# Kernel tuning notes

Hardware: AMD Instinct MI355X
Metric: run time of the kernel (lower is better)

## Reference

```python
import jax, jax.numpy as jnp
import numpy as np

N, E = 100000, 1600000
F_IN, H, HG, L, C = 128, 128, 128, 3, 40


def setup_inputs() -> dict:
    key = jax.random.key(0)
    ks = jax.random.split(key, 12)
    s = 0.05
    return dict(
        x=jax.random.normal(ks[0], (N, F_IN), jnp.float32),
        edge_index=jax.random.randint(ks[1], (2, E), 0, N),
        edge_weight=jax.random.uniform(ks[2], (E,), jnp.float32),
        h0=jax.random.normal(ks[3], (N, HG), jnp.float32),
        linW=jax.random.normal(ks[4], (F_IN, H), jnp.float32) * s,
        linB=jnp.zeros((H,), jnp.float32),
        convW=jax.random.normal(ks[5], (L, H, H), jnp.float32) * s,
        convB=jnp.zeros((L, H), jnp.float32),
        gru_Wih=jax.random.normal(ks[6], (3 * HG, H), jnp.float32) * s,
        gru_Whh=jax.random.normal(ks[7], (3 * HG, HG), jnp.float32) * s,
        gru_bih=jnp.zeros((3 * HG,), jnp.float32),
        gru_bhh=jnp.zeros((3 * HG,), jnp.float32),
        fcW=jax.random.normal(ks[8], (HG, C), jnp.float32) * s,
        fcB=jnp.zeros((C,), jnp.float32),
    )


def _gru(x, h, Wih, Whh, bih, bhh):
    # torch.nn.GRUCell math (gate order: r, z, n)
    gi = x @ Wih.T + bih  # [N, 3*HG]
    gh = h @ Whh.T + bhh  # [N, 3*HG]
    ir, iz, in_ = jnp.split(gi, 3, axis=-1)
    hr, hz, hn = jnp.split(gh, 3, axis=-1)
    r = jax.nn.sigmoid(ir + hr)
    z = jax.nn.sigmoid(iz + hz)
    n = jnp.tanh(in_ + r * hn)
    return (1.0 - z) * n + z * h


def _gcn_conv(x, src, dst, ew, W, b, n_nodes):
    # PyG GCNConv: linear -> symmetric-normalized sparse aggregation -> bias
    xw = x @ W  # [N, H]
    deg = jax.ops.segment_sum(ew, dst, num_segments=n_nodes)
    dinv = jnp.where(deg > 0, jax.lax.rsqrt(deg), 0.0)
    norm = dinv[src] * ew * dinv[dst]  # [E+N]
    msg = xw[src] * norm[:, None]      # gather + scale (irregular access)
    out = jax.ops.segment_sum(msg, dst, num_segments=n_nodes)  # scatter-add
    return out + b


def reference(x, edge_index, edge_weight, h0, linW, linB, convW, convB,
              gru_Wih, gru_Whh, gru_bih, gru_bhh, fcW, fcB):
    n_nodes = x.shape[0]
    # GCNConv default: add self-loops with weight 1 before normalization
    loops = jnp.arange(n_nodes)
    src = jnp.concatenate([edge_index[0], loops])
    dst = jnp.concatenate([edge_index[1], loops])
    ew = jnp.concatenate([edge_weight, jnp.ones((n_nodes,), edge_weight.dtype)])

    h = h0
    xh = jax.nn.relu(x @ linW + linB)
    h = _gru(xh, h, gru_Wih, gru_Whh, gru_bih, gru_bhh)
    for l in range(convW.shape[0]):  # fixed small layer count
        xh = jax.nn.relu(_gcn_conv(xh, src, dst, ew, convW[l], convB[l], n_nodes))
        h = _gru(xh, h, gru_Wih, gru_Whh, gru_bih, gru_bhh)
    return h @ fcW + fcB
```

## Files before the change

### kernel.cpp

```cpp
#include <hip/hip_runtime.h>
#include <hip/hip_bf16.h>
#include <math.h>

typedef __attribute__((ext_vector_type(8))) short bf8_t;
typedef __attribute__((ext_vector_type(4))) float f4_t;
typedef __attribute__((ext_vector_type(8))) unsigned short us8_t;

__device__ inline unsigned short f2bf(float f) {
  union { float f; unsigned u; } x; x.f = f;
  unsigned r = x.u + 0x7FFF + ((x.u >> 16) & 1);
  return (unsigned short)(r >> 16);
}
__device__ inline float bf2f(unsigned short b) {
  union { unsigned u; float f; } x; x.u = ((unsigned)b) << 16;
  return x.f;
}
__device__ inline float bflo(unsigned v) {
  union { unsigned u; float f; } x; x.u = v << 16; return x.f;
}
__device__ inline float bfhi(unsigned v) {
  union { unsigned u; float f; } x; x.u = v & 0xFFFF0000u; return x.f;
}

__device__ inline void async_copy16(const void* g, void* l) {
  __builtin_amdgcn_global_load_lds(
      (const __attribute__((address_space(1))) unsigned int*)g,
      (__attribute__((address_space(3))) unsigned int*)l, 16, 0, 0);
}


__global__ void k_zero_i(int* __restrict__ p, int n) {
  int i = blockIdx.x * blockDim.x + threadIdx.x;
  if (i < n) p[i] = 0;
}

__global__ void k_count_pos(const int* __restrict__ dst, int* __restrict__ cnt,
                            int* __restrict__ pos, int E) {
  int e = blockIdx.x * blockDim.x + threadIdx.x;
  if (e < E) pos[e] = atomicAdd(&cnt[dst[e]], 1);
}

__global__ void k_f2bf(const float* __restrict__ in, unsigned short* __restrict__ out,
                       size_t n8) {
  size_t i = (size_t)blockIdx.x * blockDim.x + threadIdx.x;
  if (i >= n8) return;
  const float4* p = (const float4*)(in + i * 8);
  float4 a = p[0], b = p[1];
  us8_t v;
  v[0] = f2bf(a.x); v[1] = f2bf(a.y); v[2] = f2bf(a.z); v[3] = f2bf(a.w);
  v[4] = f2bf(b.x); v[5] = f2bf(b.y); v[6] = f2bf(b.z); v[7] = f2bf(b.w);
  *(us8_t*)(out + i * 8) = v;
}

__global__ void k_packB(const float* __restrict__ W, unsigned short* __restrict__ out,
                        int K, int Ncols, int ldw, int trans) {
  int idx = blockIdx.x * 256 + threadIdx.x;
  int total = (Ncols / 16) * (K / 32) * 64;
  if (idx >= total) return;
  int lane = idx & 63;
  int frag = idx >> 6;
  int kt = K / 32;
  int k0 = frag % kt;
  int n0 = frag / kt;
  int n = n0 * 16 + (lane & 15);
  int kbase = k0 * 32 + (lane >> 4) * 8;
  us8_t v;
#pragma unroll
  for (int j = 0; j < 8; ++j) {
    int k = kbase + j;
    float f = trans ? W[(size_t)n * ldw + k] : W[(size_t)k * ldw + n];
    v[j] = f2bf(f);
  }
  *(us8_t*)(out + (size_t)idx * 8) = v;
}


__global__ __launch_bounds__(256) void k_scan_block(
    const int* __restrict__ cnt, int* __restrict__ partial,
    int* __restrict__ bsum, int n) {
  __shared__ int s[256];
  int tid = threadIdx.x;
  int i = blockIdx.x * 256 + tid;
  s[tid] = (i < n) ? cnt[i] : 0;
  __syncthreads();
#pragma unroll
  for (int d = 1; d < 256; d <<= 1) {
    int t = (tid >= d) ? s[tid - d] : 0;
    __syncthreads();
    s[tid] += t;
    __syncthreads();
  }
  if (i < n) partial[i] = s[tid];
  if (tid == 255) bsum[blockIdx.x] = s[255];
}

__global__ __launch_bounds__(512) void k_scan_sums(int* __restrict__ bsum, int nb) {
  __shared__ int s[512];
  int tid = threadIdx.x;
  s[tid] = (tid < nb) ? bsum[tid] : 0;
  __syncthreads();
#pragma unroll
  for (int d = 1; d < 512; d <<= 1) {
    int t = (tid >= d) ? s[tid - d] : 0;
    __syncthreads();
    s[tid] += t;
    __syncthreads();
  }
  if (tid < nb) bsum[tid] = s[tid];
}

__global__ __launch_bounds__(256) void k_scan_add(
    const int* __restrict__ partial, const int* __restrict__ bsum,
    int* __restrict__ rowptr, int n) {
  int i = blockIdx.x * 256 + threadIdx.x;
  if (i == 0) rowptr[0] = 0;
  if (i < n) {
    int v = partial[i] + (blockIdx.x > 0 ? bsum[blockIdx.x - 1] : 0);
    rowptr[i + 1] = v;
  }
}

__global__ __launch_bounds__(256) void k_csr_fill(
    const int* __restrict__ src, const int* __restrict__ dst,
    const float* __restrict__ ew, const int* __restrict__ rowptr,
    const int* __restrict__ pos, int2* __restrict__ csr, int E) {
  int e = blockIdx.x * 256 + threadIdx.x;
  if (e >= E) return;
  int d = dst[e];
  int p = rowptr[d] + pos[e];
  csr[p] = make_int2(src[e], __float_as_int(ew[e]));
}

__global__ __launch_bounds__(256) void k_deg_dinv(
    const int* __restrict__ rowptr, const int2* __restrict__ csr,
    float* __restrict__ dinv, int N) {
  int n = blockIdx.x * 256 + threadIdx.x;
  if (n >= N) return;
  int b = rowptr[n], e = rowptr[n + 1];
  float s = 1.0f;
  for (int j = b; j < e; ++j) s += __int_as_float(csr[j].y);
  dinv[n] = rsqrtf(s);
}

__global__ __launch_bounds__(256) void k_norm_csr(
    const int* __restrict__ rowptr, int2* __restrict__ csr,
    const float* __restrict__ dinv, int N) {
  int n = blockIdx.x * 256 + threadIdx.x;
  if (n >= N) return;
  int b = rowptr[n], e = rowptr[n + 1];
  float dn = dinv[n];
  for (int j = b; j < e; ++j) {
    int2 t = csr[j];
    float w = dinv[t.x] * __int_as_float(t.y) * dn;
    csr[j] = make_int2(t.x, __float_as_int(w));
  }
}


template<bool RELU, bool BIAS>
__global__ __launch_bounds__(256) void k_mfma_gemm(
    const unsigned short* __restrict__ A, const unsigned short* __restrict__ Bp,
    const float* __restrict__ bias, unsigned short* __restrict__ C, int M) {
  __shared__ unsigned char smem[32 * 1024];
  int wave = threadIdx.x >> 6, lane = threadIdx.x & 63;
  int row0 = (blockIdx.x * 4 + wave) * 16;
  int m = lane & 15, q = lane >> 4;

#pragma unroll
  for (int i = 0; i < 8; ++i) {
    int f = wave * 8 + i;
    async_copy16((const unsigned char*)Bp + (size_t)f * 1024 + lane * 16,
                 smem + f * 1024);
  }
  __syncthreads();
  if (row0 >= M) return;

  int arow = row0 + m; if (arow >= M) arow = M - 1;
  bf8_t a[4];
#pragma unroll
  for (int k0 = 0; k0 < 4; ++k0)
    a[k0] = *(const bf8_t*)(A + (size_t)arow * 128 + k0 * 32 + q * 8);

#pragma unroll
  for (int n0 = 0; n0 < 8; ++n0) {
    f4_t acc = {};
#pragma unroll
    for (int k0 = 0; k0 < 4; ++k0) {
      bf8_t b = *(const bf8_t*)(smem + (n0 * 4 + k0) * 1024 + lane * 16);
      acc = __builtin_amdgcn_mfma_f32_16x16x32_bf16(a[k0], b, acc, 0, 0, 0);
    }
    int col = n0 * 16 + m;
    float bs = BIAS ? bias[col] : 0.f;
#pragma unroll
    for (int r = 0; r < 4; ++r) {
      int grow = row0 + q * 4 + r;
      if (grow < M) {
        float v = acc[r] + bs;
        if (RELU) v = fmaxf(v, 0.f);
        C[(size_t)grow * 128 + col] = f2bf(v);
      }
    }
  }
}


__global__ __launch_bounds__(256) void k_gru_mfma(
    const unsigned short* __restrict__ xh,
    const float* h_in,
    float* h_out,
    const unsigned short* __restrict__ Bi,
    const unsigned short* __restrict__ Bh,
    const float* __restrict__ bih, const float* __restrict__ bhh, int M) {
  __shared__ unsigned char smem[24 * 1024];
  int wave = threadIdx.x >> 6, lane = threadIdx.x & 63;
  int row0 = (blockIdx.x * 4 + wave) * 16;
  int m = lane & 15, q = lane >> 4;
  int arow = row0 + m; if (arow >= M) arow = M - 1;

  bf8_t ax[4], ah[4];
#pragma unroll
  for (int k0 = 0; k0 < 4; ++k0) {
    ax[k0] = *(const bf8_t*)(xh + (size_t)arow * 128 + k0 * 32 + q * 8);
    const float* hp = h_in + (size_t)arow * 128 + k0 * 32 + q * 8;
    float4 h0 = *(const float4*)hp;
    float4 h1 = *(const float4*)(hp + 4);
    bf8_t t;
    t[0] = (short)f2bf(h0.x); t[1] = (short)f2bf(h0.y);
    t[2] = (short)f2bf(h0.z); t[3] = (short)f2bf(h0.w);
    t[4] = (short)f2bf(h1.x); t[5] = (short)f2bf(h1.y);
    t[6] = (short)f2bf(h1.z); t[7] = (short)f2bf(h1.w);
    ah[k0] = t;
  }

  auto stage = [&](int g) {
#pragma unroll
    for (int s = 0; s < 6; ++s) {
      int cc = g + 8 * (s >= 3 ? s - 3 : s);
      const unsigned short* src = (s < 3) ? Bi : Bh;
      int f = s * 4 + wave;
      async_copy16((const unsigned char*)src + ((size_t)(cc * 4 + wave)) * 1024 + lane * 16,
                   smem + f * 1024);
    }
  };

  stage(0);
  for (int g = 0; g < 8; ++g) {
    __syncthreads();
    f4_t air = {}, aiz = {}, ain = {}, ahr = {}, ahz = {}, ahn = {};
#pragma unroll
    for (int k0 = 0; k0 < 4; ++k0) {
      bf8_t br = *(const bf8_t*)(smem + (0 * 4 + k0) * 1024 + lane * 16);
      bf8_t bz = *(const bf8_t*)(smem + (1 * 4 + k0) * 1024 + lane * 16);
      bf8_t bn = *(const bf8_t*)(smem + (2 * 4 + k0) * 1024 + lane * 16);
      bf8_t cr = *(const bf8_t*)(smem + (3 * 4 + k0) * 1024 + lane * 16);
      bf8_t cz = *(const bf8_t*)(smem + (4 * 4 + k0) * 1024 + lane * 16);
      bf8_t cn = *(const bf8_t*)(smem + (5 * 4 + k0) * 1024 + lane * 16);
      air = __builtin_amdgcn_mfma_f32_16x16x32_bf16(ax[k0], br, air, 0, 0, 0);
      aiz = __builtin_amdgcn_mfma_f32_16x16x32_bf16(ax[k0], bz, aiz, 0, 0, 0);
      ain = __builtin_amdgcn_mfma_f32_16x16x32_bf16(ax[k0], bn, ain, 0, 0, 0);
      ahr = __builtin_amdgcn_mfma_f32_16x16x32_bf16(ah[k0], cr, ahr, 0, 0, 0);
      ahz = __builtin_amdgcn_mfma_f32_16x16x32_bf16(ah[k0], cz, ahz, 0, 0, 0);
      ahn = __builtin_amdgcn_mfma_f32_16x16x32_bf16(ah[k0], cn, ahn, 0, 0, 0);
    }
    __syncthreads();
    if (g < 7) stage(g + 1);

    int col = g * 16 + m;
    float bir_ = bih[col], biz_ = bih[col + 128], bin_ = bih[col + 256];
    float bhr_ = bhh[col], bhz_ = bhh[col + 128], bhn_ = bhh[col + 256];
#pragma unroll
    for (int r = 0; r < 4; ++r) {
      int grow = row0 + q * 4 + r;
      if (grow < M) {
        float hprev = h_in[(size_t)grow * 128 + col];
        float rr = 1.f / (1.f + expf(-(air[r] + bir_ + ahr[r] + bhr_)));
        float zz = 1.f / (1.f + expf(-(aiz[r] + biz_ + ahz[r] + bhz_)));
        float nn = tanhf(ain[r] + bin_ + rr * (ahn[r] + bhn_));
        h_out[(size_t)grow * 128 + col] = (1.f - zz) * nn + zz * hprev;
      }
    }
  }
}


template<bool RELU, bool BIAS>
__global__ __launch_bounds__(256) void k_gemm128(
    const float* __restrict__ A, const float* __restrict__ B,
    const float* __restrict__ bias, float* __restrict__ C, int M, int Nc) {
  __shared__ float As[64][36];
  __shared__ float Bs[32][64];
  int tid = threadIdx.x;
  int tx = tid & 15, ty = tid >> 4;
  int row0 = blockIdx.y * 64, col0 = blockIdx.x * 64;
  float acc[4][4] = {};

  for (int k0 = 0; k0 < 128; k0 += 32) {
#pragma unroll
    for (int i = 0; i < 2; ++i) {
      int f = tid + i * 256;
      int r = f >> 3, c4 = f & 7;
      int gr = row0 + r;
      float4 v = make_float4(0.f, 0.f, 0.f, 0.f);
      if (gr < M) v = *(const float4*)(A + (size_t)gr * 128 + k0 + c4 * 4);
      *(float4*)(&As[r][c4 * 4]) = v;
    }
#pragma unroll
    for (int i = 0; i < 2; ++i) {
      int f = tid + i * 256;
      int r = f >> 4, c4 = f & 15;
      int gc = col0 + c4 * 4;
      float4 v = make_float4(0.f, 0.f, 0.f, 0.f);
      if (gc + 3 < Nc) v = *(const float4*)(B + (size_t)(k0 + r) * Nc + gc);
      *(float4*)(&Bs[r][c4 * 4]) = v;
    }
    __syncthreads();
#pragma unroll
    for (int kk = 0; kk < 32; ++kk) {
      float4 b = *(float4*)(&Bs[kk][tx * 4]);
      float a0 = As[ty * 4 + 0][kk];
      float a1 = As[ty * 4 + 1][kk];
      float a2 = As[ty * 4 + 2][kk];
      float a3 = As[ty * 4 + 3][kk];
      acc[0][0] += a0 * b.x; acc[0][1] += a0 * b.y; acc[0][2] += a0 * b.z; acc[0][3] += a0 * b.w;
      acc[1][0] += a1 * b.x; acc[1][1] += a1 * b.y; acc[1][2] += a1 * b.z; acc[1][3] += a1 * b.w;
      acc[2][0] += a2 * b.x; acc[2][1] += a2 * b.y; acc[2][2] += a2 * b.z; acc[2][3] += a2 * b.w;
      acc[3][0] += a3 * b.x; acc[3][1] += a3 * b.y; acc[3][2] += a3 * b.z; acc[3][3] += a3 * b.w;
    }
    __syncthreads();
  }

#pragma unroll
  for (int i = 0; i < 4; ++i) {
    int gr = row0 + ty * 4 + i;
    if (gr >= M) continue;
#pragma unroll
    for (int j = 0; j < 4; ++j) {
      int gc = col0 + tx * 4 + j;
      if (gc >= Nc) continue;
      float v = acc[i][j];
      if (BIAS) v += bias[gc];
      if (RELU) v = fmaxf(v, 0.f);
      C[(size_t)gr * Nc + gc] = v;
    }
  }
}


__global__ __launch_bounds__(256) void k_gather(
    const int* __restrict__ rowptr, const int2* __restrict__ csr,
    const unsigned* __restrict__ xw,
    const float* __restrict__ dinv, const float* __restrict__ bias,
    unsigned* __restrict__ out, int N) {
  int wave = threadIdx.x >> 6;
  int lane = threadIdx.x & 63;
  int node = __builtin_amdgcn_readfirstlane(blockIdx.x * 4 + wave);
  if (node >= N) return;
  int beg = __builtin_amdgcn_readfirstlane(rowptr[node]);
  int end = __builtin_amdgcn_readfirstlane(rowptr[node + 1]);

  float accl = 0.f, acch = 0.f;
  int k = beg;
  for (; k + 4 <= end; k += 4) {
    int2 e0 = csr[k], e1 = csr[k + 1], e2 = csr[k + 2], e3 = csr[k + 3];
    unsigned v0 = xw[((size_t)e0.x << 6) + lane];
    unsigned v1 = xw[((size_t)e1.x << 6) + lane];
    unsigned v2 = xw[((size_t)e2.x << 6) + lane];
    unsigned v3 = xw[((size_t)e3.x << 6) + lane];
    float w0 = __int_as_float(e0.y), w1 = __int_as_float(e1.y);
    float w2 = __int_as_float(e2.y), w3 = __int_as_float(e3.y);
    accl += bflo(v0) * w0; acch += bfhi(v0) * w0;
    accl += bflo(v1) * w1; acch += bfhi(v1) * w1;
    accl += bflo(v2) * w2; acch += bfhi(v2) * w2;
    accl += bflo(v3) * w3; acch += bfhi(v3) * w3;
  }
  for (; k < end; ++k) {
    int2 e = csr[k];
    unsigned v = xw[((size_t)e.x << 6) + lane];
    float w = __int_as_float(e.y);
    accl += bflo(v) * w; acch += bfhi(v) * w;
  }

  float di = dinv[node];
  float sn = di * di;
  unsigned vs = xw[((size_t)node << 6) + lane];
  float2 b = *(const float2*)(bias + lane * 2);
  float rl = fmaxf(accl + bflo(vs) * sn + b.x, 0.f);
  float rh = fmaxf(acch + bfhi(vs) * sn + b.y, 0.f);
  unsigned o = (unsigned)f2bf(rl) | ((unsigned)f2bf(rh) << 16);
  out[((size_t)node << 6) + lane] = o;
}


extern "C" void kernel_launch(void* const* d_in, const int* in_sizes, int n_in,
                              void* d_out, int out_size, void* d_ws, size_t ws_size,
                              hipStream_t stream) {
  const float* x    = (const float*)d_in[0];
  const int*   ei   = (const int*)d_in[1];
  const float* ew   = (const float*)d_in[2];
  const float* h0   = (const float*)d_in[3];
  const float* linW = (const float*)d_in[4];
  const float* linB = (const float*)d_in[5];
  const float* convW= (const float*)d_in[6];
  const float* convB= (const float*)d_in[7];
  const float* Wih  = (const float*)d_in[8];
  const float* Whh  = (const float*)d_in[9];
  const float* bih  = (const float*)d_in[10];
  const float* bhh  = (const float*)d_in[11];
  const float* fcW  = (const float*)d_in[12];
  const float* fcB  = (const float*)d_in[13];

  int N = in_sizes[0] / 128;
  int E = in_sizes[1] / 2;
  const int* srcI = ei;
  const int* dstI = ei + E;
  int nb = (N + 255) / 256;

  float* ws = (float*)d_ws;
  size_t off = 0;
  float* dinv = ws + off; off += (size_t)N;
  if (off & 1) off++;
  float* h    = ws + off; off += (size_t)N * 128;
  int* iws = (int*)(ws + off);
  size_t ioff = 0;
  int2* csr    = (int2*)iws; ioff += (size_t)2 * E;
  int* cnt     = iws + ioff; ioff += (size_t)N;
  int* partial = iws + ioff; ioff += (size_t)N;
  int* bsum    = iws + ioff; ioff += 512;
  int* rowptr  = iws + ioff; ioff += (size_t)N + 1;
  ioff = (ioff + 3) & ~(size_t)3;
  unsigned short* usws = (unsigned short*)(iws + ioff);
  size_t uoff = 0;
  unsigned short* x_bf   = usws + uoff; uoff += (size_t)N * 128;
  unsigned short* xh_bf  = usws + uoff; uoff += (size_t)N * 128;
  unsigned short* xw_bf  = usws + uoff; uoff += (size_t)N * 128;
  unsigned short* linWp  = usws + uoff; uoff += 128 * 128;
  unsigned short* convWp = usws + uoff; uoff += 3 * 128 * 128;
  unsigned short* Bi     = usws + uoff; uoff += 384 * 128;
  unsigned short* Bh     = usws + uoff; uoff += 384 * 128;

  int* pos = (int*)xw_bf;

  k_packB<<<(8 * 4 * 64 + 255) / 256, 256, 0, stream>>>(linW, linWp, 128, 128, 128, 0);
  for (int l = 0; l < 3; ++l)
    k_packB<<<(8 * 4 * 64 + 255) / 256, 256, 0, stream>>>(
        convW + (size_t)l * 128 * 128, convWp + (size_t)l * 128 * 128, 128, 128, 128, 0);
  k_packB<<<(24 * 4 * 64 + 255) / 256, 256, 0, stream>>>(Wih, Bi, 128, 384, 128, 1);
  k_packB<<<(24 * 4 * 64 + 255) / 256, 256, 0, stream>>>(Whh, Bh, 128, 384, 128, 1);

  k_f2bf<<<(int)(((size_t)N * 16 + 255) / 256), 256, 0, stream>>>(x, x_bf, (size_t)N * 16);

  k_zero_i<<<nb, 256, 0, stream>>>(cnt, N);
  k_count_pos<<<(E + 255) / 256, 256, 0, stream>>>(dstI, cnt, pos, E);
  k_scan_block<<<nb, 256, 0, stream>>>(cnt, partial, bsum, N);
  k_scan_sums<<<1, 512, 0, stream>>>(bsum, nb);
  k_scan_add<<<nb, 256, 0, stream>>>(partial, bsum, rowptr, N);
  k_csr_fill<<<(E + 255) / 256, 256, 0, stream>>>(
      srcI, dstI, ew, rowptr, pos, csr, E);

  k_deg_dinv<<<nb, 256, 0, stream>>>(rowptr, csr, dinv, N);
  k_norm_csr<<<nb, 256, 0, stream>>>(rowptr, csr, dinv, N);

  int gwave = (N + 63) / 64;

  k_mfma_gemm<true, true><<<gwave, 256, 0, stream>>>(x_bf, linWp, linB, xh_bf, N);

  k_gru_mfma<<<gwave, 256, 0, stream>>>(xh_bf, h0, h, Bi, Bh, bih, bhh, N);

  int ggat = (N + 3) / 4;
  for (int l = 0; l < 3; ++l) {
    k_mfma_gemm<false, false><<<gwave, 256, 0, stream>>>(
        xh_bf, convWp + (size_t)l * 128 * 128, nullptr, xw_bf, N);
    k_gather<<<ggat, 256, 0, stream>>>(
        rowptr, csr, (const unsigned*)xw_bf, dinv, convB + (size_t)l * 128,
        (unsigned*)xh_bf, N);
    k_gru_mfma<<<gwave, 256, 0, stream>>>(xh_bf, h, h, Bi, Bh, bih, bhh, N);
  }

  dim3 g40(1, (N + 63) / 64);
  k_gemm128<false, true><<<g40, 256, 0, stream>>>(h, fcW, fcB, (float*)d_out, N, 40);
}
```

Measured before the change: 914.2 us.

## Fuse gather with GRU and merge independent setup kernels by block-range dispatch

The sparse aggregation is fused into the GRU kernel. Each wave gathers 16 nodes, writes the bf16 rows into swizzled LDS, and feeds them straight to the MFMA GRU, so the xh round trip through global memory disappears and the last layer skips writing xh entirely. Independent setup steps (weight packing with count zeroing, edge counting with f32-to-bf16 conversion, CSR fill with the input linear, degree with the first GRU, normalisation with the first conv GEMM) are merged into single launches that split work by block index. CSR accesses also switch to nontemporal loads and stores. The gather now runs serially over 16 nodes per wave instead of one node per wave, which cuts parallelism and latency hiding in the irregular gather phase.

```diff
diff --git a/kernel.cpp b/kernel.cpp
--- a/kernel.cpp
+++ b/kernel.cpp
@@ -11,10 +11,6 @@
   unsigned r = x.u + 0x7FFF + ((x.u >> 16) & 1);
   return (unsigned short)(r >> 16);
 }
-__device__ inline float bf2f(unsigned short b) {
-  union { unsigned u; float f; } x; x.u = ((unsigned)b) << 16;
-  return x.f;
-}
 __device__ inline float bflo(unsigned v) {
   union { unsigned u; float f; } x; x.u = v << 16; return x.f;
 }
@@ -29,32 +25,10 @@
 }
 
 
-__global__ void k_zero_i(int* __restrict__ p, int n) {
-  int i = blockIdx.x * blockDim.x + threadIdx.x;
-  if (i < n) p[i] = 0;
-}
-
-__global__ void k_count_pos(const int* __restrict__ dst, int* __restrict__ cnt,
-                            int* __restrict__ pos, int E) {
-  int e = blockIdx.x * blockDim.x + threadIdx.x;
-  if (e < E) pos[e] = atomicAdd(&cnt[dst[e]], 1);
-}
-
-__global__ void k_f2bf(const float* __restrict__ in, unsigned short* __restrict__ out,
-                       size_t n8) {
-  size_t i = (size_t)blockIdx.x * blockDim.x + threadIdx.x;
-  if (i >= n8) return;
-  const float4* p = (const float4*)(in + i * 8);
-  float4 a = p[0], b = p[1];
-  us8_t v;
-  v[0] = f2bf(a.x); v[1] = f2bf(a.y); v[2] = f2bf(a.z); v[3] = f2bf(a.w);
-  v[4] = f2bf(b.x); v[5] = f2bf(b.y); v[6] = f2bf(b.z); v[7] = f2bf(b.w);
-  *(us8_t*)(out + i * 8) = v;
-}
-
-__global__ void k_packB(const float* __restrict__ W, unsigned short* __restrict__ out,
-                        int K, int Ncols, int ldw, int trans) {
-  int idx = blockIdx.x * 256 + threadIdx.x;
+__device__ inline void packB_body(const float* __restrict__ W,
+                                  unsigned short* __restrict__ out,
+                                  int K, int Ncols, int ldw, int trans, int bid) {
+  int idx = bid * 256 + threadIdx.x;
   int total = (Ncols / 16) * (K / 32) * 64;
   if (idx >= total) return;
   int lane = idx & 63;
@@ -74,96 +48,55 @@
   *(us8_t*)(out + (size_t)idx * 8) = v;
 }
 
-
-__global__ __launch_bounds__(256) void k_scan_block(
-    const int* __restrict__ cnt, int* __restrict__ partial,
-    int* __restrict__ bsum, int n) {
-  __shared__ int s[256];
-  int tid = threadIdx.x;
-  int i = blockIdx.x * 256 + tid;
-  s[tid] = (i < n) ? cnt[i] : 0;
-  __syncthreads();
-#pragma unroll
-  for (int d = 1; d < 256; d <<= 1) {
-    int t = (tid >= d) ? s[tid - d] : 0;
-    __syncthreads();
-    s[tid] += t;
-    __syncthreads();
-  }
-  if (i < n) partial[i] = s[tid];
-  if (tid == 255) bsum[blockIdx.x] = s[255];
-}
-
-__global__ __launch_bounds__(512) void k_scan_sums(int* __restrict__ bsum, int nb) {
-  __shared__ int s[512];
-  int tid = threadIdx.x;
-  s[tid] = (tid < nb) ? bsum[tid] : 0;
-  __syncthreads();
-#pragma unroll
-  for (int d = 1; d < 512; d <<= 1) {
-    int t = (tid >= d) ? s[tid - d] : 0;
-    __syncthreads();
-    s[tid] += t;
-    __syncthreads();
-  }
-  if (tid < nb) bsum[tid] = s[tid];
-}
-
-__global__ __launch_bounds__(256) void k_scan_add(
-    const int* __restrict__ partial, const int* __restrict__ bsum,
-    int* __restrict__ rowptr, int n) {
-  int i = blockIdx.x * 256 + threadIdx.x;
-  if (i == 0) rowptr[0] = 0;
-  if (i < n) {
-    int v = partial[i] + (blockIdx.x > 0 ? bsum[blockIdx.x - 1] : 0);
-    rowptr[i + 1] = v;
-  }
-}
-
-__global__ __launch_bounds__(256) void k_csr_fill(
-    const int* __restrict__ src, const int* __restrict__ dst,
-    const float* __restrict__ ew, const int* __restrict__ rowptr,
-    const int* __restrict__ pos, int2* __restrict__ csr, int E) {
-  int e = blockIdx.x * 256 + threadIdx.x;
+__device__ inline void fill_body(const int* __restrict__ src, const int* __restrict__ dst,
+                                 const float* __restrict__ ew, const int* __restrict__ rowptr,
+                                 const int* __restrict__ pos, int2* __restrict__ csr,
+                                 int E, int bid) {
+  int e = bid * 256 + threadIdx.x;
   if (e >= E) return;
   int d = dst[e];
   int p = rowptr[d] + pos[e];
-  csr[p] = make_int2(src[e], __float_as_int(ew[e]));
-}
-
-__global__ __launch_bounds__(256) void k_deg_dinv(
-    const int* __restrict__ rowptr, const int2* __restrict__ csr,
-    float* __restrict__ dinv, int N) {
-  int n = blockIdx.x * 256 + threadIdx.x;
+  unsigned long long v = (unsigned long long)(unsigned)src[e] |
+                         ((unsigned long long)(unsigned)__float_as_int(ew[e]) << 32);
+  __builtin_nontemporal_store(v, (unsigned long long*)(csr + p));
+}
+
+__device__ inline void deg_body(const int* __restrict__ rowptr, const int2* __restrict__ csr,
+                                float* __restrict__ dinv, int N, int bid) {
+  int n = bid * 256 + threadIdx.x;
   if (n >= N) return;
   int b = rowptr[n], e = rowptr[n + 1];
   float s = 1.0f;
-  for (int j = b; j < e; ++j) s += __int_as_float(csr[j].y);
+  for (int j = b; j < e; ++j) {
+    unsigned long long v = __builtin_nontemporal_load((const unsigned long long*)(csr + j));
+    s += __int_as_float((int)(v >> 32));
+  }
   dinv[n] = rsqrtf(s);
 }
 
-__global__ __launch_bounds__(256) void k_norm_csr(
-    const int* __restrict__ rowptr, int2* __restrict__ csr,
-    const float* __restrict__ dinv, int N) {
-  int n = blockIdx.x * 256 + threadIdx.x;
+__device__ inline void norm_body(const int* __restrict__ rowptr, int2* __restrict__ csr,
+                                 const float* __restrict__ dinv, int N, int bid) {
+  int n = bid * 256 + threadIdx.x;
   if (n >= N) return;
   int b = rowptr[n], e = rowptr[n + 1];
   float dn = dinv[n];
   for (int j = b; j < e; ++j) {
-    int2 t = csr[j];
-    float w = dinv[t.x] * __int_as_float(t.y) * dn;
-    csr[j] = make_int2(t.x, __float_as_int(w));
-  }
-}
-
-
-template<bool RELU, bool BIAS>
-__global__ __launch_bounds__(256) void k_mfma_gemm(
-    const unsigned short* __restrict__ A, const unsigned short* __restrict__ Bp,
-    const float* __restrict__ bias, unsigned short* __restrict__ C, int M) {
-  __shared__ unsigned char smem[32 * 1024];
+    unsigned long long v = __builtin_nontemporal_load((const unsigned long long*)(csr + j));
+    int s = (int)v;
+    float w = dinv[s] * __int_as_float((int)(v >> 32)) * dn;
+    unsigned long long nv = (unsigned long long)(unsigned)s |
+                            ((unsigned long long)(unsigned)__float_as_int(w) << 32);
+    __builtin_nontemporal_store(nv, (unsigned long long*)(csr + j));
+  }
+}
+
+__device__ inline void gemm_body(const unsigned short* __restrict__ A,
+                                 const unsigned short* __restrict__ Bp,
+                                 const float* __restrict__ bias,
+                                 unsigned short* __restrict__ C, int M, int bid,
+                                 bool relu, bool hasbias, unsigned char* smem) {
   int wave = threadIdx.x >> 6, lane = threadIdx.x & 63;
-  int row0 = (blockIdx.x * 4 + wave) * 16;
+  int row0 = (bid * 4 + wave) * 16;
   int m = lane & 15, q = lane >> 4;
 
 #pragma unroll
@@ -190,37 +123,43 @@
       acc = __builtin_amdgcn_mfma_f32_16x16x32_bf16(a[k0], b, acc, 0, 0, 0);
     }
     int col = n0 * 16 + m;
-    float bs = BIAS ? bias[col] : 0.f;
+    float bs = hasbias ? bias[col] : 0.f;
 #pragma unroll
     for (int r = 0; r < 4; ++r) {
       int grow = row0 + q * 4 + r;
       if (grow < M) {
         float v = acc[r] + bs;
-        if (RELU) v = fmaxf(v, 0.f);
+        if (relu) v = fmaxf(v, 0.f);
         C[(size_t)grow * 128 + col] = f2bf(v);
       }
     }
   }
 }
 
-
-__global__ __launch_bounds__(256) void k_gru_mfma(
-    const unsigned short* __restrict__ xh,
-    const float* h_in,
-    float* h_out,
-    const unsigned short* __restrict__ Bi,
-    const unsigned short* __restrict__ Bh,
-    const float* __restrict__ bih, const float* __restrict__ bhh, int M) {
-  __shared__ unsigned char smem[24 * 1024];
-  int wave = threadIdx.x >> 6, lane = threadIdx.x & 63;
-  int row0 = (blockIdx.x * 4 + wave) * 16;
+__device__ inline void gru_stage(const unsigned short* __restrict__ Bi,
+                                 const unsigned short* __restrict__ Bh,
+                                 unsigned char* smem, int wave, int lane, int g) {
+#pragma unroll
+  for (int s = 0; s < 6; ++s) {
+    int cc = g + 8 * (s >= 3 ? s - 3 : s);
+    const unsigned short* src = (s < 3) ? Bi : Bh;
+    int f = s * 4 + wave;
+    async_copy16((const unsigned char*)src + ((size_t)(cc * 4 + wave)) * 1024 + lane * 16,
+                 smem + f * 1024);
+  }
+}
+
+__device__ inline void gru_core(const bf8_t* ax, const float* h_in, float* h_out,
+                                const unsigned short* __restrict__ Bi,
+                                const unsigned short* __restrict__ Bh,
+                                const float* __restrict__ bih, const float* __restrict__ bhh,
+                                int M, int row0, int wave, int lane, unsigned char* smem) {
   int m = lane & 15, q = lane >> 4;
   int arow = row0 + m; if (arow >= M) arow = M - 1;
 
-  bf8_t ax[4], ah[4];
+  bf8_t ah[4];
 #pragma unroll
   for (int k0 = 0; k0 < 4; ++k0) {
-    ax[k0] = *(const bf8_t*)(xh + (size_t)arow * 128 + k0 * 32 + q * 8);
     const float* hp = h_in + (size_t)arow * 128 + k0 * 32 + q * 8;
     float4 h0 = *(const float4*)hp;
     float4 h1 = *(const float4*)(hp + 4);
@@ -232,18 +171,6 @@
     ah[k0] = t;
   }
 
-  auto stage = [&](int g) {
-#pragma unroll
-    for (int s = 0; s < 6; ++s) {
-      int cc = g + 8 * (s >= 3 ? s - 3 : s);
-      const unsigned short* src = (s < 3) ? Bi : Bh;
-      int f = s * 4 + wave;
-      async_copy16((const unsigned char*)src + ((size_t)(cc * 4 + wave)) * 1024 + lane * 16,
-                   smem + f * 1024);
-    }
-  };
-
-  stage(0);
   for (int g = 0; g < 8; ++g) {
     __syncthreads();
     f4_t air = {}, aiz = {}, ain = {}, ahr = {}, ahz = {}, ahn = {};
@@ -263,7 +190,7 @@
       ahn = __builtin_amdgcn_mfma_f32_16x16x32_bf16(ah[k0], cn, ahn, 0, 0, 0);
     }
     __syncthreads();
-    if (g < 7) stage(g + 1);
+    if (g < 7) gru_stage(Bi, Bh, smem, wave, lane, g + 1);
 
     int col = g * 16 + m;
     float bir_ = bih[col], biz_ = bih[col + 128], bin_ = bih[col + 256];
@@ -280,6 +207,220 @@
       }
     }
   }
+}
+
+
+__global__ __launch_bounds__(256) void k_prep(
+    const float* __restrict__ linW, const float* __restrict__ convW,
+    const float* __restrict__ Wih, const float* __restrict__ Whh,
+    unsigned short* __restrict__ linWp, unsigned short* __restrict__ convWp,
+    unsigned short* __restrict__ Bi, unsigned short* __restrict__ Bh,
+    int* __restrict__ cnt, int N) {
+  int b = blockIdx.x;
+  if (b < 8)  { packB_body(linW, linWp, 128, 128, 128, 0, b); return; }
+  if (b < 32) { int l = (b - 8) >> 3;
+                packB_body(convW + (size_t)l * 16384, convWp + (size_t)l * 16384,
+                           128, 128, 128, 0, (b - 8) & 7); return; }
+  if (b < 56) { packB_body(Wih, Bi, 128, 384, 128, 1, b - 32); return; }
+  if (b < 80) { packB_body(Whh, Bh, 128, 384, 128, 1, b - 56); return; }
+  int i = (b - 80) * 256 + threadIdx.x;
+  if (i < N) cnt[i] = 0;
+}
+
+__global__ __launch_bounds__(256) void k_count_f2bf(
+    const int* __restrict__ dst, int* __restrict__ cnt, int* __restrict__ pos, int E,
+    const float* __restrict__ xin, unsigned short* __restrict__ xout, size_t n8,
+    int nCnt) {
+  if ((int)blockIdx.x < nCnt) {
+    int e = blockIdx.x * 256 + threadIdx.x;
+    if (e < E) pos[e] = atomicAdd(&cnt[dst[e]], 1);
+    return;
+  }
+  size_t i = (size_t)(blockIdx.x - nCnt) * 256 + threadIdx.x;
+  if (i >= n8) return;
+  const float4* p = (const float4*)(xin + i * 8);
+  float4 a = p[0], b = p[1];
+  us8_t v;
+  v[0] = f2bf(a.x); v[1] = f2bf(a.y); v[2] = f2bf(a.z); v[3] = f2bf(a.w);
+  v[4] = f2bf(b.x); v[5] = f2bf(b.y); v[6] = f2bf(b.z); v[7] = f2bf(b.w);
+  *(us8_t*)(xout + i * 8) = v;
+}
+
+__global__ __launch_bounds__(256) void k_scan_block(
+    const int* __restrict__ cnt, int* __restrict__ partial,
+    int* __restrict__ bsum, int n) {
+  __shared__ int s[256];
+  int tid = threadIdx.x;
+  int i = blockIdx.x * 256 + tid;
+  s[tid] = (i < n) ? cnt[i] : 0;
+  __syncthreads();
+#pragma unroll
+  for (int d = 1; d < 256; d <<= 1) {
+    int t = (tid >= d) ? s[tid - d] : 0;
+    __syncthreads();
+    s[tid] += t;
+    __syncthreads();
+  }
+  if (i < n) partial[i] = s[tid];
+  if (tid == 255) bsum[blockIdx.x] = s[255];
+}
+
+__global__ __launch_bounds__(512) void k_scan_sums(int* __restrict__ bsum, int nb) {
+  __shared__ int s[512];
+  int tid = threadIdx.x;
+  s[tid] = (tid < nb) ? bsum[tid] : 0;
+  __syncthreads();
+#pragma unroll
+  for (int d = 1; d < 512; d <<= 1) {
+    int t = (tid >= d) ? s[tid - d] : 0;
+    __syncthreads();
+    s[tid] += t;
+    __syncthreads();
+  }
+  if (tid < nb) bsum[tid] = s[tid];
+}
+
+__global__ __launch_bounds__(256) void k_scan_add(
+    const int* __restrict__ partial, const int* __restrict__ bsum,
+    int* __restrict__ rowptr, int n) {
+  int i = blockIdx.x * 256 + threadIdx.x;
+  if (i == 0) rowptr[0] = 0;
+  if (i < n) {
+    int v = partial[i] + (blockIdx.x > 0 ? bsum[blockIdx.x - 1] : 0);
+    rowptr[i + 1] = v;
+  }
+}
+
+__global__ __launch_bounds__(256) void k_fill_lin(
+    const int* __restrict__ src, const int* __restrict__ dstI,
+    const float* __restrict__ ew, const int* __restrict__ rowptr,
+    const int* __restrict__ pos, int2* __restrict__ csr, int E,
+    const unsigned short* __restrict__ A, const unsigned short* __restrict__ Bp,
+    const float* __restrict__ bias, unsigned short* __restrict__ C, int M,
+    int nFill) {
+  __shared__ unsigned char smem[32 * 1024];
+  if ((int)blockIdx.x < nFill) {
+    fill_body(src, dstI, ew, rowptr, pos, csr, E, blockIdx.x);
+    return;
+  }
+  gemm_body(A, Bp, bias, C, M, blockIdx.x - nFill, true, true, smem);
+}
+
+__global__ __launch_bounds__(256) void k_deg_gru(
+    const int* __restrict__ rowptr, const int2* __restrict__ csr,
+    float* __restrict__ dinv, int N,
+    const unsigned short* __restrict__ xh, const float* h_in, float* h_out,
+    const unsigned short* __restrict__ Bi, const unsigned short* __restrict__ Bh,
+    const float* __restrict__ bih, const float* __restrict__ bhh, int M,
+    int nDeg) {
+  __shared__ unsigned char smem[24 * 1024];
+  if ((int)blockIdx.x < nDeg) {
+    deg_body(rowptr, csr, dinv, N, blockIdx.x);
+    return;
+  }
+  int bid = blockIdx.x - nDeg;
+  int wave = threadIdx.x >> 6, lane = threadIdx.x & 63;
+  int row0 = (bid * 4 + wave) * 16;
+  gru_stage(Bi, Bh, smem, wave, lane, 0);
+  int m = lane & 15, q = lane >> 4;
+  int arow = row0 + m; if (arow >= M) arow = M - 1;
+  bf8_t ax[4];
+#pragma unroll
+  for (int k0 = 0; k0 < 4; ++k0)
+    ax[k0] = *(const bf8_t*)(xh + (size_t)arow * 128 + k0 * 32 + q * 8);
+  gru_core(ax, h_in, h_out, Bi, Bh, bih, bhh, M, row0, wave, lane, smem);
+}
+
+__global__ __launch_bounds__(256) void k_norm_conv(
+    const int* __restrict__ rowptr, int2* __restrict__ csr,
+    const float* __restrict__ dinv, int N,
+    const unsigned short* __restrict__ A, const unsigned short* __restrict__ Bp,
+    unsigned short* __restrict__ C, int M, int nNorm) {
+  __shared__ unsigned char smem[32 * 1024];
+  if ((int)blockIdx.x < nNorm) {
+    norm_body(rowptr, csr, dinv, N, blockIdx.x);
+    return;
+  }
+  gemm_body(A, Bp, nullptr, C, M, blockIdx.x - nNorm, false, false, smem);
+}
+
+template<bool RELU, bool BIAS>
+__global__ __launch_bounds__(256) void k_mfma_gemm(
+    const unsigned short* __restrict__ A, const unsigned short* __restrict__ Bp,
+    const float* __restrict__ bias, unsigned short* __restrict__ C, int M) {
+  __shared__ unsigned char smem[32 * 1024];
+  gemm_body(A, Bp, bias, C, M, blockIdx.x, RELU, BIAS, smem);
+}
+
+
+template<bool WRITE_XH>
+__global__ __launch_bounds__(256) void k_gather_gru(
+    const int* __restrict__ rowptr, const int2* __restrict__ csr,
+    const unsigned* __restrict__ xw,
+    const float* __restrict__ dinv, const float* __restrict__ bias,
+    const float* h_in, float* h_out,
+    const unsigned short* __restrict__ Bi, const unsigned short* __restrict__ Bh,
+    const float* __restrict__ bih, const float* __restrict__ bhh,
+    unsigned* __restrict__ xh_out, int M) {
+  __shared__ unsigned char smem[24 * 1024];
+  __shared__ unsigned char rows_[4][16 * 256];
+  int wave = threadIdx.x >> 6, lane = threadIdx.x & 63;
+  int row0 = (blockIdx.x * 4 + wave) * 16;
+
+  gru_stage(Bi, Bh, smem, wave, lane, 0);
+
+  float2 bb = *(const float2*)(bias + lane * 2);
+
+  for (int j = 0; j < 16; ++j) {
+    int node = row0 + j;
+    unsigned o = 0u;
+    if (node < M) {
+      int beg = __builtin_amdgcn_readfirstlane(rowptr[node]);
+      int end = __builtin_amdgcn_readfirstlane(rowptr[node + 1]);
+      float accl = 0.f, acch = 0.f;
+      int k = beg;
+      for (; k + 4 <= end; k += 4) {
+        unsigned long long r0 = __builtin_nontemporal_load((const unsigned long long*)(csr + k));
+        unsigned long long r1 = __builtin_nontemporal_load((const unsigned long long*)(csr + k + 1));
+        unsigned long long r2 = __builtin_nontemporal_load((const unsigned long long*)(csr + k + 2));
+        unsigned long long r3 = __builtin_nontemporal_load((const unsigned long long*)(csr + k + 3));
+        unsigned v0 = xw[((size_t)(unsigned)r0 << 6) + lane];
+        unsigned v1 = xw[((size_t)(unsigned)r1 << 6) + lane];
+        unsigned v2 = xw[((size_t)(unsigned)r2 << 6) + lane];
+        unsigned v3 = xw[((size_t)(unsigned)r3 << 6) + lane];
+        float w0 = __int_as_float((int)(r0 >> 32)), w1 = __int_as_float((int)(r1 >> 32));
+        float w2 = __int_as_float((int)(r2 >> 32)), w3 = __int_as_float((int)(r3 >> 32));
+        accl += bflo(v0) * w0; acch += bfhi(v0) * w0;
+        accl += bflo(v1) * w1; acch += bfhi(v1) * w1;
+        accl += bflo(v2) * w2; acch += bfhi(v2) * w2;
+        accl += bflo(v3) * w3; acch += bfhi(v3) * w3;
+      }
+      for (; k < end; ++k) {
+        unsigned long long r = __builtin_nontemporal_load((const unsigned long long*)(csr + k));
+        unsigned v = xw[((size_t)(unsigned)r << 6) + lane];
+        float w = __int_as_float((int)(r >> 32));
+        accl += bflo(v) * w; acch += bfhi(v) * w;
+      }
+      float di = dinv[node];
+      float sn = di * di;
+      unsigned vs = xw[((size_t)node << 6) + lane];
+      float rl = fmaxf(accl + bflo(vs) * sn + bb.x, 0.f);
+      float rh = fmaxf(acch + bfhi(vs) * sn + bb.y, 0.f);
+      o = (unsigned)f2bf(rl) | ((unsigned)f2bf(rh) << 16);
+      if (WRITE_XH) xh_out[((size_t)node << 6) + lane] = o;
+    }
+    unsigned byteoff = ((unsigned)(lane * 4)) ^ (((unsigned)(j & 7)) << 4);
+    *(unsigned*)(&rows_[wave][j * 256] + byteoff) = o;
+  }
+
+  int m = lane & 15, q = lane >> 4;
+  bf8_t ax[4];
+#pragma unroll
+  for (int k0 = 0; k0 < 4; ++k0) {
+    unsigned rb = ((unsigned)(k0 * 64 + q * 16)) ^ (((unsigned)(m & 7)) << 4);
+    ax[k0] = *(const bf8_t*)(&rows_[wave][m * 256] + rb);
+  }
+  gru_core(ax, h_in, h_out, Bi, Bh, bih, bhh, M, row0, wave, lane, smem);
 }
 
 
@@ -343,51 +484,6 @@
       C[(size_t)gr * Nc + gc] = v;
     }
   }
-}
-
-
-__global__ __launch_bounds__(256) void k_gather(
-    const int* __restrict__ rowptr, const int2* __restrict__ csr,
-    const unsigned* __restrict__ xw,
-    const float* __restrict__ dinv, const float* __restrict__ bias,
-    unsigned* __restrict__ out, int N) {
-  int wave = threadIdx.x >> 6;
-  int lane = threadIdx.x & 63;
-  int node = __builtin_amdgcn_readfirstlane(blockIdx.x * 4 + wave);
-  if (node >= N) return;
-  int beg = __builtin_amdgcn_readfirstlane(rowptr[node]);
-  int end = __builtin_amdgcn_readfirstlane(rowptr[node + 1]);
-
-  float accl = 0.f, acch = 0.f;
-  int k = beg;
-  for (; k + 4 <= end; k += 4) {
-    int2 e0 = csr[k], e1 = csr[k + 1], e2 = csr[k + 2], e3 = csr[k + 3];
-    unsigned v0 = xw[((size_t)e0.x << 6) + lane];
-    unsigned v1 = xw[((size_t)e1.x << 6) + lane];
-    unsigned v2 = xw[((size_t)e2.x << 6) + lane];
-    unsigned v3 = xw[((size_t)e3.x << 6) + lane];
-    float w0 = __int_as_float(e0.y), w1 = __int_as_float(e1.y);
-    float w2 = __int_as_float(e2.y), w3 = __int_as_float(e3.y);
-    accl += bflo(v0) * w0; acch += bfhi(v0) * w0;
-    accl += bflo(v1) * w1; acch += bfhi(v1) * w1;
-    accl += bflo(v2) * w2; acch += bfhi(v2) * w2;
-    accl += bflo(v3) * w3; acch += bfhi(v3) * w3;
-  }
-  for (; k < end; ++k) {
-    int2 e = csr[k];
-    unsigned v = xw[((size_t)e.x << 6) + lane];
-    float w = __int_as_float(e.y);
-    accl += bflo(v) * w; acch += bfhi(v) * w;
-  }
-
-  float di = dinv[node];
-  float sn = di * di;
-  unsigned vs = xw[((size_t)node << 6) + lane];
-  float2 b = *(const float2*)(bias + lane * 2);
-  float rl = fmaxf(accl + bflo(vs) * sn + b.x, 0.f);
-  float rh = fmaxf(acch + bfhi(vs) * sn + b.y, 0.f);
-  unsigned o = (unsigned)f2bf(rl) | ((unsigned)f2bf(rh) << 16);
-  out[((size_t)node << 6) + lane] = o;
 }
 
 
@@ -440,42 +536,36 @@
 
   int* pos = (int*)xw_bf;
 
-  k_packB<<<(8 * 4 * 64 + 255) / 256, 256, 0, stream>>>(linW, linWp, 128, 128, 128, 0);
-  for (int l = 0; l < 3; ++l)
-    k_packB<<<(8 * 4 * 64 + 255) / 256, 256, 0, stream>>>(
-        convW + (size_t)l * 128 * 128, convWp + (size_t)l * 128 * 128, 128, 128, 128, 0);
-  k_packB<<<(24 * 4 * 64 + 255) / 256, 256, 0, stream>>>(Wih, Bi, 128, 384, 128, 1);
-  k_packB<<<(24 * 4 * 64 + 255) / 256, 256, 0, stream>>>(Whh, Bh, 128, 384, 128, 1);
-
-  k_f2bf<<<(int)(((size_t)N * 16 + 255) / 256), 256, 0, stream>>>(x, x_bf, (size_t)N * 16);
-
-  k_zero_i<<<nb, 256, 0, stream>>>(cnt, N);
-  k_count_pos<<<(E + 255) / 256, 256, 0, stream>>>(dstI, cnt, pos, E);
+  int gwave = (N + 63) / 64;
+  int nCnt  = (E + 255) / 256;
+  int nF2   = (int)(((size_t)N * 16 + 255) / 256);
+
+  k_prep<<<80 + nb, 256, 0, stream>>>(linW, convW, Wih, Whh,
+                                      linWp, convWp, Bi, Bh, cnt, N);
+  k_count_f2bf<<<nCnt + nF2, 256, 0, stream>>>(dstI, cnt, pos, E,
+                                               x, x_bf, (size_t)N * 16, nCnt);
   k_scan_block<<<nb, 256, 0, stream>>>(cnt, partial, bsum, N);
   k_scan_sums<<<1, 512, 0, stream>>>(bsum, nb);
   k_scan_add<<<nb, 256, 0, stream>>>(partial, bsum, rowptr, N);
-  k_csr_fill<<<(E + 255) / 256, 256, 0, stream>>>(
-      srcI, dstI, ew, rowptr, pos, csr, E);
-
-  k_deg_dinv<<<nb, 256, 0, stream>>>(rowptr, csr, dinv, N);
-  k_norm_csr<<<nb, 256, 0, stream>>>(rowptr, csr, dinv, N);
-
-  int gwave = (N + 63) / 64;
-
-  k_mfma_gemm<true, true><<<gwave, 256, 0, stream>>>(x_bf, linWp, linB, xh_bf, N);
-
-  k_gru_mfma<<<gwave, 256, 0, stream>>>(xh_bf, h0, h, Bi, Bh, bih, bhh, N);
-
-  int ggat = (N + 3) / 4;
-  for (int l = 0; l < 3; ++l) {
-    k_mfma_gemm<false, false><<<gwave, 256, 0, stream>>>(
-        xh_bf, convWp + (size_t)l * 128 * 128, nullptr, xw_bf, N);
-    k_gather<<<ggat, 256, 0, stream>>>(
-        rowptr, csr, (const unsigned*)xw_bf, dinv, convB + (size_t)l * 128,
-        (unsigned*)xh_bf, N);
-    k_gru_mfma<<<gwave, 256, 0, stream>>>(xh_bf, h, h, Bi, Bh, bih, bhh, N);
-  }
-
+  k_fill_lin<<<nCnt + gwave, 256, 0, stream>>>(srcI, dstI, ew, rowptr, pos, csr, E,
+                                               x_bf, linWp, linB, xh_bf, N, nCnt);
+  k_deg_gru<<<nb + gwave, 256, 0, stream>>>(rowptr, csr, dinv, N,
+                                            xh_bf, h0, h, Bi, Bh, bih, bhh, N, nb);
+  k_norm_conv<<<nb + gwave, 256, 0, stream>>>(rowptr, csr, dinv, N,
+                                              xh_bf, convWp, xw_bf, N, nb);
+  k_gather_gru<true><<<gwave, 256, 0, stream>>>(
+      rowptr, csr, (const unsigned*)xw_bf, dinv, convB,
+      h, h, Bi, Bh, bih, bhh, (unsigned*)xh_bf, N);
+  k_mfma_gemm<false, false><<<gwave, 256, 0, stream>>>(
+      xh_bf, convWp + (size_t)1 * 128 * 128, nullptr, xw_bf, N);
+  k_gather_gru<true><<<gwave, 256, 0, stream>>>(
+      rowptr, csr, (const unsigned*)xw_bf, dinv, convB + 128,
+      h, h, Bi, Bh, bih, bhh, (unsigned*)xh_bf, N);
+  k_mfma_gemm<false, false><<<gwave, 256, 0, stream>>>(
+      xh_bf, convWp + (size_t)2 * 128 * 128, nullptr, xw_bf, N);
+  k_gather_gru<false><<<gwave, 256, 0, stream>>>(
+      rowptr, csr, (const unsigned*)xw_bf, dinv, convB + 256,
+      h, h, Bi, Bh, bih, bhh, nullptr, N);
   dim3 g40(1, (N + 63) / 64);
   k_gemm128<false, true><<<g40, 256, 0, stream>>>(h, fcW, fcB, (float*)d_out, N, 40);
 }
```

Result: slower. 986.4 us (+7.9%).
